# Kernel tuning notes

Hardware: AMD Instinct MI355X
Metric: run time of the kernel (lower is better)

## Reference

```python
import jax, jax.numpy as jnp
import numpy as np

N_NODES = 50000
N_EDGES = 800000
D_IN = 128
D_OUT = 64

def setup_inputs() -> dict:
    key = jax.random.key(0)
    k1, k2, k3, k4 = jax.random.split(key, 4)
    X = jax.random.normal(k1, (N_NODES, D_IN), dtype=jnp.float32)
    # match torch init: uniform(-stdv, stdv), stdv = 1/sqrt(output_dim)
    stdv = 1.0 / np.sqrt(D_OUT)
    weights = jax.random.uniform(k2, (D_IN, D_OUT), dtype=jnp.float32, minval=-stdv, maxval=stdv)
    # CSR-equivalent edge list: sorted row ids (destination/aggregating node) + column ids (neighbor)
    row_index = jnp.sort(jax.random.randint(k3, (N_EDGES,), 0, N_NODES, dtype=jnp.int32))
    column_index = jax.random.randint(k4, (N_EDGES,), 0, N_NODES, dtype=jnp.int32)
    return {"X": X, "weights": weights, "row_index": row_index, "column_index": column_index}

def reference(X, weights, row_index, column_index):
    # Dense transform: [N, D_in] @ [D_in, D_out] -> [N, D_out]
    X_prime = X @ weights
    # TCGNN CSR SpMM aggregation (unweighted neighbor sum):
    # out[i] = sum_{e: row[e]==i} X_prime[col[e]]
    gathered = X_prime[column_index]  # [E, D_out]
    out = jax.ops.segment_sum(gathered, row_index, num_segments=N_NODES)
    return out
```

## Files before the change

### kernel.cpp

```cpp
#include <hip/hip_runtime.h>
#include <hip/hip_bf16.h>

#define N_NODES 50000
#define D_IN    128
#define D_OUT   64
#define N_EDGES 800000
#define GROWS   64

__global__ __launch_bounds__(256, 2) void gemm_xw(const float* __restrict__ X,
                                                  const float* __restrict__ W,
                                                  float* __restrict__ Xp) {
    __shared__ float Xs[GROWS][D_IN + 4];
    __shared__ float Ws[D_IN][D_OUT];

    const int tid  = threadIdx.x;
    const int row0 = blockIdx.x * GROWS;

    {
        const float4* W4  = reinterpret_cast<const float4*>(W);
        float4*       Ws4 = reinterpret_cast<float4*>(&Ws[0][0]);
        #pragma unroll
        for (int t = 0; t < 8; ++t) Ws4[tid + 256 * t] = W4[tid + 256 * t];
    }
    {
        const float4* X4 = reinterpret_cast<const float4*>(X);
        #pragma unroll
        for (int t = 0; t < 8; ++t) {
            const int s  = tid + 256 * t;
            const int r  = s >> 5;
            const int kq = s & 31;
            const int gr = row0 + r;
            float4 v = make_float4(0.f, 0.f, 0.f, 0.f);
            if (gr < N_NODES) v = X4[(size_t)gr * (D_IN / 4) + kq];
            *reinterpret_cast<float4*>(&Xs[r][kq * 4]) = v;
        }
    }
    __syncthreads();

    const int tc = tid & 15;
    const int tg = tid >> 4;
    const int c0 = tc * 4;
    const int r0 = tg * 4;

    float acc[4][4];
    #pragma unroll
    for (int r = 0; r < 4; ++r)
        #pragma unroll
        for (int c = 0; c < 4; ++c) acc[r][c] = 0.f;

    #pragma unroll 4
    for (int kq = 0; kq < 32; ++kq) {
        const int k0 = kq * 4;
        float4 xa[4], wb[4];
        #pragma unroll
        for (int r = 0; r < 4; ++r)
            xa[r] = *reinterpret_cast<const float4*>(&Xs[r0 + r][k0]);
        #pragma unroll
        for (int kk = 0; kk < 4; ++kk)
            wb[kk] = *reinterpret_cast<const float4*>(&Ws[k0 + kk][c0]);
        #pragma unroll
        for (int r = 0; r < 4; ++r) {
            const float x0 = xa[r].x, x1 = xa[r].y, x2 = xa[r].z, x3 = xa[r].w;
            acc[r][0] += x0 * wb[0].x + x1 * wb[1].x + x2 * wb[2].x + x3 * wb[3].x;
            acc[r][1] += x0 * wb[0].y + x1 * wb[1].y + x2 * wb[2].y + x3 * wb[3].y;
            acc[r][2] += x0 * wb[0].z + x1 * wb[1].z + x2 * wb[2].z + x3 * wb[3].z;
            acc[r][3] += x0 * wb[0].w + x1 * wb[1].w + x2 * wb[2].w + x3 * wb[3].w;
        }
    }

    #pragma unroll
    for (int r = 0; r < 4; ++r) {
        const int gr = row0 + r0 + r;
        if (gr < N_NODES) {
            float4 v = make_float4(acc[r][0], acc[r][1], acc[r][2], acc[r][3]);
            *reinterpret_cast<float4*>(&Xp[(size_t)gr * D_OUT + c0]) = v;
        }
    }
}

__global__ __launch_bounds__(256) void build_rowptr(const int* __restrict__ row,
                                                    int* __restrict__ rowptr) {
    const int i = blockIdx.x * 256 + threadIdx.x;
    if (i > N_NODES) return;
    int lo = 0, hi = N_EDGES;
    while (lo < hi) {
        int mid = (lo + hi) >> 1;
        if (row[mid] < i) lo = mid + 1; else hi = mid;
    }
    rowptr[i] = lo;
}

__global__ __launch_bounds__(256) void aggregate(const float* __restrict__ Xp,
                                                 const int* __restrict__ col,
                                                 const int* __restrict__ rowptr,
                                                 float* __restrict__ out) {
    const int wid = (blockIdx.x * 256 + threadIdx.x) >> 6;
    const int j   = threadIdx.x & 63;

    const int lo = rowptr[wid];
    const int hi = rowptr[wid + 1];

    float acc = 0.f;
    int e = lo;
    for (; e + 16 <= hi; e += 16) {
        float v[16];
        #pragma unroll
        for (int q = 0; q < 16; ++q) v[q] = Xp[(size_t)col[e + q] * D_OUT + j];
        acc += (((v[0] + v[1]) + (v[2] + v[3])) + ((v[4] + v[5]) + (v[6] + v[7])))
             + (((v[8] + v[9]) + (v[10] + v[11])) + ((v[12] + v[13]) + (v[14] + v[15])));
    }
    for (; e + 4 <= hi; e += 4) {
        float v0 = Xp[(size_t)col[e + 0] * D_OUT + j];
        float v1 = Xp[(size_t)col[e + 1] * D_OUT + j];
        float v2 = Xp[(size_t)col[e + 2] * D_OUT + j];
        float v3 = Xp[(size_t)col[e + 3] * D_OUT + j];
        acc += (v0 + v1) + (v2 + v3);
    }
    for (; e < hi; ++e) {
        acc += Xp[(size_t)col[e] * D_OUT + j];
    }
    out[(size_t)wid * D_OUT + j] = acc;
}

extern "C" void kernel_launch(void* const* d_in, const int* in_sizes, int n_in,
                              void* d_out, int out_size, void* d_ws, size_t ws_size,
                              hipStream_t stream) {
    const float* X   = (const float*)d_in[0];
    const float* W   = (const float*)d_in[1];
    const int*   row = (const int*)d_in[2];
    const int*   col = (const int*)d_in[3];
    float*       out = (float*)d_out;

    float* Xp     = (float*)d_ws;
    int*   rowptr = (int*)((char*)d_ws + (size_t)N_NODES * D_OUT * sizeof(float));

    hipLaunchKernelGGL(gemm_xw, dim3((N_NODES + GROWS - 1) / GROWS), dim3(256), 0, stream,
                       X, W, Xp);
    hipLaunchKernelGGL(build_rowptr, dim3((N_NODES + 1 + 255) / 256), dim3(256), 0, stream,
                       row, rowptr);
    hipLaunchKernelGGL(aggregate, dim3((N_NODES * 64) / 256), dim3(256), 0, stream,
                       Xp, col, rowptr, out);
}
```

Measured before the change: 129.9 us.

## Store transformed features in fp16 and retile GEMM to 128-row blocks

The intermediate X@W matrix is now written as fp16 and the aggregation kernel gathers half-precision values, converting them to float before accumulating. This halves the bytes moved by the gather-heavy SpMM and by the intermediate write. The GEMM is also retiled to 128 rows per block with 4x8 outputs per thread, loading X in two K halves so shared memory stays small. The risk is reduced precision in the intermediate values. In the aggregate kernel each lane now reads a 2-byte element, so a wavefront fetches 128 contiguous bytes per row.

```diff
diff --git a/kernel.cpp b/kernel.cpp
--- a/kernel.cpp
+++ b/kernel.cpp
@@ -1,20 +1,22 @@
 #include <hip/hip_runtime.h>
 #include <hip/hip_bf16.h>
+#include <hip/hip_fp16.h>
 
 #define N_NODES 50000
 #define D_IN    128
 #define D_OUT   64
 #define N_EDGES 800000
-#define GROWS   64
+#define BROWS   128
+#define XS_LD   68
 
 __global__ __launch_bounds__(256, 2) void gemm_xw(const float* __restrict__ X,
                                                   const float* __restrict__ W,
-                                                  float* __restrict__ Xp) {
-    __shared__ float Xs[GROWS][D_IN + 4];
+                                                  __half* __restrict__ Xp) {
+    __shared__ float Xs[BROWS][XS_LD];
     __shared__ float Ws[D_IN][D_OUT];
 
     const int tid  = threadIdx.x;
-    const int row0 = blockIdx.x * GROWS;
+    const int row0 = blockIdx.x * BROWS;
 
     {
         const float4* W4  = reinterpret_cast<const float4*>(W);
@@ -22,58 +24,69 @@
         #pragma unroll
         for (int t = 0; t < 8; ++t) Ws4[tid + 256 * t] = W4[tid + 256 * t];
     }
-    {
-        const float4* X4 = reinterpret_cast<const float4*>(X);
+
+    const int colg = tid & 7;
+    const int rowg = tid >> 3;
+    const int c0   = colg * 8;
+
+    float acc[4][8];
+    #pragma unroll
+    for (int r = 0; r < 4; ++r)
+        #pragma unroll
+        for (int c = 0; c < 8; ++c) acc[r][c] = 0.f;
+
+    const float4* X4 = reinterpret_cast<const float4*>(X);
+
+    for (int h = 0; h < 2; ++h) {
+        __syncthreads();
         #pragma unroll
         for (int t = 0; t < 8; ++t) {
             const int s  = tid + 256 * t;
-            const int r  = s >> 5;
-            const int kq = s & 31;
+            const int r  = s >> 4;
+            const int q  = s & 15;
             const int gr = row0 + r;
             float4 v = make_float4(0.f, 0.f, 0.f, 0.f);
-            if (gr < N_NODES) v = X4[(size_t)gr * (D_IN / 4) + kq];
-            *reinterpret_cast<float4*>(&Xs[r][kq * 4]) = v;
+            if (gr < N_NODES) v = X4[(size_t)gr * 32 + h * 16 + q];
+            *reinterpret_cast<float4*>(&Xs[r][q * 4]) = v;
         }
-    }
-    __syncthreads();
+        __syncthreads();
 
-    const int tc = tid & 15;
-    const int tg = tid >> 4;
-    const int c0 = tc * 4;
-    const int r0 = tg * 4;
-
-    float acc[4][4];
-    #pragma unroll
-    for (int r = 0; r < 4; ++r)
         #pragma unroll
-        for (int c = 0; c < 4; ++c) acc[r][c] = 0.f;
-
-    #pragma unroll 4
-    for (int kq = 0; kq < 32; ++kq) {
-        const int k0 = kq * 4;
-        float4 xa[4], wb[4];
-        #pragma unroll
-        for (int r = 0; r < 4; ++r)
-            xa[r] = *reinterpret_cast<const float4*>(&Xs[r0 + r][k0]);
-        #pragma unroll
-        for (int kk = 0; kk < 4; ++kk)
-            wb[kk] = *reinterpret_cast<const float4*>(&Ws[k0 + kk][c0]);
-        #pragma unroll
-        for (int r = 0; r < 4; ++r) {
-            const float x0 = xa[r].x, x1 = xa[r].y, x2 = xa[r].z, x3 = xa[r].w;
-            acc[r][0] += x0 * wb[0].x + x1 * wb[1].x + x2 * wb[2].x + x3 * wb[3].x;
-            acc[r][1] += x0 * wb[0].y + x1 * wb[1].y + x2 * wb[2].y + x3 * wb[3].y;
-            acc[r][2] += x0 * wb[0].z + x1 * wb[1].z + x2 * wb[2].z + x3 * wb[3].z;
-            acc[r][3] += x0 * wb[0].w + x1 * wb[1].w + x2 * wb[2].w + x3 * wb[3].w;
+        for (int kq = 0; kq < 16; ++kq) {
+            const int k0 = kq * 4;
+            float4 xa[4], wb0[4], wb1[4];
+            #pragma unroll
+            for (int r = 0; r < 4; ++r)
+                xa[r] = *reinterpret_cast<const float4*>(&Xs[rowg + 32 * r][k0]);
+            #pragma unroll
+            for (int kk = 0; kk < 4; ++kk) {
+                wb0[kk] = *reinterpret_cast<const float4*>(&Ws[h * 64 + k0 + kk][c0]);
+                wb1[kk] = *reinterpret_cast<const float4*>(&Ws[h * 64 + k0 + kk][c0 + 4]);
+            }
+            #pragma unroll
+            for (int r = 0; r < 4; ++r) {
+                const float x0 = xa[r].x, x1 = xa[r].y, x2 = xa[r].z, x3 = xa[r].w;
+                acc[r][0] += x0 * wb0[0].x + x1 * wb0[1].x + x2 * wb0[2].x + x3 * wb0[3].x;
+                acc[r][1] += x0 * wb0[0].y + x1 * wb0[1].y + x2 * wb0[2].y + x3 * wb0[3].y;
+                acc[r][2] += x0 * wb0[0].z + x1 * wb0[1].z + x2 * wb0[2].z + x3 * wb0[3].z;
+                acc[r][3] += x0 * wb0[0].w + x1 * wb0[1].w + x2 * wb0[2].w + x3 * wb0[3].w;
+                acc[r][4] += x0 * wb1[0].x + x1 * wb1[1].x + x2 * wb1[2].x + x3 * wb1[3].x;
+                acc[r][5] += x0 * wb1[0].y + x1 * wb1[1].y + x2 * wb1[2].y + x3 * wb1[3].y;
+                acc[r][6] += x0 * wb1[0].z + x1 * wb1[1].z + x2 * wb1[2].z + x3 * wb1[3].z;
+                acc[r][7] += x0 * wb1[0].w + x1 * wb1[1].w + x2 * wb1[2].w + x3 * wb1[3].w;
+            }
         }
     }
 
     #pragma unroll
     for (int r = 0; r < 4; ++r) {
-        const int gr = row0 + r0 + r;
+        const int gr = row0 + rowg + 32 * r;
         if (gr < N_NODES) {
-            float4 v = make_float4(acc[r][0], acc[r][1], acc[r][2], acc[r][3]);
-            *reinterpret_cast<float4*>(&Xp[(size_t)gr * D_OUT + c0]) = v;
+            __half hbuf[8];
+            #pragma unroll
+            for (int c = 0; c < 8; ++c) hbuf[c] = __float2half(acc[r][c]);
+            *reinterpret_cast<float4*>(&Xp[(size_t)gr * D_OUT + c0]) =
+                *reinterpret_cast<float4*>(hbuf);
         }
     }
 }
@@ -90,7 +103,7 @@
     rowptr[i] = lo;
 }
 
-__global__ __launch_bounds__(256) void aggregate(const float* __restrict__ Xp,
+__global__ __launch_bounds__(256) void aggregate(const __half* __restrict__ Xp,
                                                  const int* __restrict__ col,
                                                  const int* __restrict__ rowptr,
                                                  float* __restrict__ out) {
@@ -105,19 +118,20 @@
     for (; e + 16 <= hi; e += 16) {
         float v[16];
         #pragma unroll
-        for (int q = 0; q < 16; ++q) v[q] = Xp[(size_t)col[e + q] * D_OUT + j];
+        for (int q = 0; q < 16; ++q)
+            v[q] = __half2float(Xp[(size_t)col[e + q] * D_OUT + j]);
         acc += (((v[0] + v[1]) + (v[2] + v[3])) + ((v[4] + v[5]) + (v[6] + v[7])))
              + (((v[8] + v[9]) + (v[10] + v[11])) + ((v[12] + v[13]) + (v[14] + v[15])));
     }
     for (; e + 4 <= hi; e += 4) {
-        float v0 = Xp[(size_t)col[e + 0] * D_OUT + j];
-        float v1 = Xp[(size_t)col[e + 1] * D_OUT + j];
-        float v2 = Xp[(size_t)col[e + 2] * D_OUT + j];
-        float v3 = Xp[(size_t)col[e + 3] * D_OUT + j];
+        float v0 = __half2float(Xp[(size_t)col[e + 0] * D_OUT + j]);
+        float v1 = __half2float(Xp[(size_t)col[e + 1] * D_OUT + j]);
+        float v2 = __half2float(Xp[(size_t)col[e + 2] * D_OUT + j]);
+        float v3 = __half2float(Xp[(size_t)col[e + 3] * D_OUT + j]);
         acc += (v0 + v1) + (v2 + v3);
     }
     for (; e < hi; ++e) {
-        acc += Xp[(size_t)col[e] * D_OUT + j];
+        acc += __half2float(Xp[(size_t)col[e] * D_OUT + j]);
     }
     out[(size_t)wid * D_OUT + j] = acc;
 }
@@ -131,10 +145,10 @@
     const int*   col = (const int*)d_in[3];
     float*       out = (float*)d_out;
 
-    float* Xp     = (float*)d_ws;
-    int*   rowptr = (int*)((char*)d_ws + (size_t)N_NODES * D_OUT * sizeof(float));
+    __half* Xp     = (__half*)d_ws;
+    int*    rowptr = (int*)((char*)d_ws + (size_t)N_NODES * D_OUT * sizeof(__half));
 
-    hipLaunchKernelGGL(gemm_xw, dim3((N_NODES + GROWS - 1) / GROWS), dim3(256), 0, stream,
+    hipLaunchKernelGGL(gemm_xw, dim3((N_NODES + BROWS - 1) / BROWS), dim3(256), 0, stream,
                        X, W, Xp);
     hipLaunchKernelGGL(build_rowptr, dim3((N_NODES + 1 + 255) / 256), dim3(256), 0, stream,
                        row, rowptr);
```

After: 350.4 us. 170% more time.
